# Kernel tuning notes

Measured on AMD Instinct MI355X. Metric: run time of the kernel, lower is better.

The kernel has to match this reference:

```python
import jax, jax.numpy as jnp
import numpy as np
from itertools import permutations

N_SOURCES = 5
BATCH = 524288
# All n! permutations as one-hot matrices: PERM_ONEHOT[p, i, j] = 1 iff perm p maps row i -> col j.
# Brute-force min over all permutations is exactly the Hungarian (linear_sum_assignment) optimum.
_PERMS = np.array(list(permutations(range(N_SOURCES))), dtype=np.int32)        # [120, 5]
PERM_ONEHOT = np.eye(N_SOURCES, dtype=np.float32)[_PERMS]                      # [120, 5, 5]


def setup_inputs() -> dict:
    key = jax.random.key(0)
    k1, k2 = jax.random.split(key)
    doa_predictions = jax.random.normal(k1, (BATCH, N_SOURCES), dtype=jnp.float32)
    doa_targets = jax.random.normal(k2, (BATCH, N_SOURCES), dtype=jnp.float32)
    return {"doa_predictions": doa_predictions, "doa_targets": doa_targets}


def reference(doa_predictions, doa_targets):
    n = doa_predictions.shape[1]
    # pairwise mod-pi differences, wrapped into [-pi/2, pi/2): [B, n_pred, n_tgt]
    diff = doa_predictions[:, :, None] - doa_targets[:, None, :]
    diff = (diff + jnp.pi / 2) % jnp.pi - jnp.pi / 2
    cost = diff * diff                                                   # [B, n, n]
    # total squared error under each permutation: [B, P]
    perm_costs = jnp.einsum('bij,pij->bp', cost, jnp.asarray(PERM_ONEHOT))
    min_cost = jnp.min(perm_costs, axis=1)                               # optimal assignment cost per sample
    rmspe = jnp.sqrt(min_cost / n)
    return jnp.sum(rmspe)
```

## Files before the change

kernel.cpp:

```cpp
#include <hip/hip_runtime.h>
#include <math.h>


#define NSRC 5

__device__ __forceinline__ float sample_rmspe(const float pr[NSRC], const float tg[NSRC]) {
    const float PI     = 3.14159265358979323846f;
    const float INV_PI = 0.31830988618379067154f;

    float c[NSRC][NSRC];
#pragma unroll
    for (int i = 0; i < NSRC; ++i) {
#pragma unroll
        for (int j = 0; j < NSRC; ++j) {
            float x = pr[i] - tg[j];
            float d = x - PI * floorf(fmaf(x, INV_PI, 0.5f));
            c[i][j] = d * d;
        }
    }

    float dp[1 << NSRC];
    dp[0] = 0.0f;
#pragma unroll
    for (int mask = 1; mask < (1 << NSRC); ++mask) {
        const int i = __popc(mask) - 1;
        float best = 3.4e38f;
#pragma unroll
        for (int j = 0; j < NSRC; ++j) {
            if (mask & (1 << j)) {
                float cand = dp[mask ^ (1 << j)] + c[i][j];
                best = fminf(best, cand);
            }
        }
        dp[mask] = best;
    }
    return sqrtf(dp[(1 << NSRC) - 1] * (1.0f / NSRC));
}

__global__ __launch_bounds__(256) void rmspe_partial(const float4* __restrict__ pred4,
                                                     const float4* __restrict__ tgt4,
                                                     float* __restrict__ partial,
                                                     int nquad, int B,
                                                     const float* __restrict__ pred,
                                                     const float* __restrict__ tgt) {
    float val = 0.0f;
    const int stride = gridDim.x * blockDim.x;
    for (int q = blockIdx.x * blockDim.x + threadIdx.x; q < nquad; q += stride) {
        const float4* pp = pred4 + (size_t)q * NSRC;
        const float4* tp = tgt4  + (size_t)q * NSRC;
        float4 p0 = pp[0], p1 = pp[1], p2 = pp[2], p3 = pp[3], p4 = pp[4];
        float4 t0 = tp[0], t1 = tp[1], t2 = tp[2], t3 = tp[3], t4 = tp[4];
        float pf[20] = {p0.x,p0.y,p0.z,p0.w, p1.x,p1.y,p1.z,p1.w,
                        p2.x,p2.y,p2.z,p2.w, p3.x,p3.y,p3.z,p3.w,
                        p4.x,p4.y,p4.z,p4.w};
        float tf[20] = {t0.x,t0.y,t0.z,t0.w, t1.x,t1.y,t1.z,t1.w,
                        t2.x,t2.y,t2.z,t2.w, t3.x,t3.y,t3.z,t3.w,
                        t4.x,t4.y,t4.z,t4.w};
#pragma unroll
        for (int s = 0; s < 4; ++s)
            val += sample_rmspe(&pf[s * NSRC], &tf[s * NSRC]);
    }

    const int tail_start = nquad * 4;
    const int gtid = blockIdx.x * blockDim.x + threadIdx.x;
    if (tail_start + gtid < B) {
        float pr[NSRC], tg[NSRC];
#pragma unroll
        for (int i = 0; i < NSRC; ++i) {
            pr[i] = pred[(size_t)(tail_start + gtid) * NSRC + i];
            tg[i] = tgt [(size_t)(tail_start + gtid) * NSRC + i];
        }
        val += sample_rmspe(pr, tg);
    }

#pragma unroll
    for (int off = 32; off > 0; off >>= 1)
        val += __shfl_down(val, off, 64);

    __shared__ float wsum[4];
    const int lane = threadIdx.x & 63;
    const int wid  = threadIdx.x >> 6;
    if (lane == 0) wsum[wid] = val;
    __syncthreads();
    if (threadIdx.x == 0)
        partial[blockIdx.x] = wsum[0] + wsum[1] + wsum[2] + wsum[3];
}

__global__ __launch_bounds__(256) void rmspe_reduce(const float* __restrict__ partial,
                                                    int n, float* __restrict__ out) {
    float v = 0.0f;
    for (int i = threadIdx.x; i < n; i += 256) v += partial[i];
#pragma unroll
    for (int off = 32; off > 0; off >>= 1)
        v += __shfl_down(v, off, 64);
    __shared__ float wsum[4];
    const int lane = threadIdx.x & 63;
    const int wid  = threadIdx.x >> 6;
    if (lane == 0) wsum[wid] = v;
    __syncthreads();
    if (threadIdx.x == 0)
        out[0] = wsum[0] + wsum[1] + wsum[2] + wsum[3];
}

extern "C" void kernel_launch(void* const* d_in, const int* in_sizes, int n_in,
                              void* d_out, int out_size, void* d_ws, size_t ws_size,
                              hipStream_t stream) {
    const float* pred = (const float*)d_in[0];
    const float* tgt  = (const float*)d_in[1];
    float* out = (float*)d_out;
    float* partial = (float*)d_ws;

    const int B = in_sizes[0] / NSRC;
    const int nquad = B / 4;

    const int threads = 256;
    int blocks = (nquad + threads - 1) / threads;
    if (blocks > 2048) blocks = 2048;
    if (blocks < 1) blocks = 1;

    rmspe_partial<<<blocks, threads, 0, stream>>>(
        (const float4*)pred, (const float4*)tgt, partial, nquad, B, pred, tgt);
    rmspe_reduce<<<1, threads, 0, stream>>>(partial, blocks, out);
}
```

Measured before the change: 11.86 us.

## Prescale inputs by 1/pi and wrap with hardware fract; shrink grid and reducer

Inputs are pre-scaled by 1/pi once per element, with the +0.5 offset folded into predictions, so each of the 25 pairwise wraps becomes a hardware fract minus 0.5. The squared-cost scale (pi^2/n) moves into a single multiply before a native sqrt per sample. This removes per-pair floor and multiply work from the ALU-bound inner loop. The grid is capped at 512 blocks so each thread handles more quads, and the final reducer becomes a single wave with no shared memory. Fract-based wrapping may differ slightly in rounding from the floor-based modulo near wrap boundaries.

```diff
diff --git a/kernel.cpp b/kernel.cpp
--- a/kernel.cpp
+++ b/kernel.cpp
@@ -4,18 +4,15 @@
 
 #define NSRC 5
 
-__device__ __forceinline__ float sample_rmspe(const float pr[NSRC], const float tg[NSRC]) {
-    const float PI     = 3.14159265358979323846f;
-    const float INV_PI = 0.31830988618379067154f;
-
+__device__ __forceinline__ float sample_dp(const float u[NSRC], const float v[NSRC]) {
     float c[NSRC][NSRC];
 #pragma unroll
     for (int i = 0; i < NSRC; ++i) {
 #pragma unroll
         for (int j = 0; j < NSRC; ++j) {
-            float x = pr[i] - tg[j];
-            float d = x - PI * floorf(fmaf(x, INV_PI, 0.5f));
-            c[i][j] = d * d;
+            float t = u[i] - v[j];
+            float g = __builtin_amdgcn_fractf(t) - 0.5f;
+            c[i][j] = g * g;
         }
     }
 
@@ -34,7 +31,7 @@
         }
         dp[mask] = best;
     }
-    return sqrtf(dp[(1 << NSRC) - 1] * (1.0f / NSRC));
+    return dp[(1 << NSRC) - 1];
 }
 
 __global__ __launch_bounds__(256) void rmspe_partial(const float4* __restrict__ pred4,
@@ -43,6 +40,9 @@
                                                      int nquad, int B,
                                                      const float* __restrict__ pred,
                                                      const float* __restrict__ tgt) {
+    const float INV_PI = 0.31830988618379067154f;
+    const float PI2_OVER_N = 1.9739208802178717f;
+
     float val = 0.0f;
     const int stride = gridDim.x * blockDim.x;
     for (int q = blockIdx.x * blockDim.x + threadIdx.x; q < nquad; q += stride) {
@@ -57,20 +57,27 @@
                         t2.x,t2.y,t2.z,t2.w, t3.x,t3.y,t3.z,t3.w,
                         t4.x,t4.y,t4.z,t4.w};
 #pragma unroll
-        for (int s = 0; s < 4; ++s)
-            val += sample_rmspe(&pf[s * NSRC], &tf[s * NSRC]);
+        for (int k = 0; k < 20; ++k) {
+            pf[k] = fmaf(pf[k], INV_PI, 0.5f);
+            tf[k] = tf[k] * INV_PI;
+        }
+#pragma unroll
+        for (int s = 0; s < 4; ++s) {
+            float m = sample_dp(&pf[s * NSRC], &tf[s * NSRC]);
+            val += __builtin_amdgcn_sqrtf(m * PI2_OVER_N);
+        }
     }
 
     const int tail_start = nquad * 4;
     const int gtid = blockIdx.x * blockDim.x + threadIdx.x;
     if (tail_start + gtid < B) {
-        float pr[NSRC], tg[NSRC];
+        float u[NSRC], v[NSRC];
 #pragma unroll
         for (int i = 0; i < NSRC; ++i) {
-            pr[i] = pred[(size_t)(tail_start + gtid) * NSRC + i];
-            tg[i] = tgt [(size_t)(tail_start + gtid) * NSRC + i];
+            u[i] = fmaf(pred[(size_t)(tail_start + gtid) * NSRC + i], INV_PI, 0.5f);
+            v[i] = tgt [(size_t)(tail_start + gtid) * NSRC + i] * INV_PI;
         }
-        val += sample_rmspe(pr, tg);
+        val += __builtin_amdgcn_sqrtf(sample_dp(u, v) * PI2_OVER_N);
     }
 
 #pragma unroll
@@ -86,20 +93,14 @@
         partial[blockIdx.x] = wsum[0] + wsum[1] + wsum[2] + wsum[3];
 }
 
-__global__ __launch_bounds__(256) void rmspe_reduce(const float* __restrict__ partial,
-                                                    int n, float* __restrict__ out) {
+__global__ __launch_bounds__(64) void rmspe_reduce(const float* __restrict__ partial,
+                                                   int n, float* __restrict__ out) {
     float v = 0.0f;
-    for (int i = threadIdx.x; i < n; i += 256) v += partial[i];
+    for (int i = threadIdx.x; i < n; i += 64) v += partial[i];
 #pragma unroll
     for (int off = 32; off > 0; off >>= 1)
         v += __shfl_down(v, off, 64);
-    __shared__ float wsum[4];
-    const int lane = threadIdx.x & 63;
-    const int wid  = threadIdx.x >> 6;
-    if (lane == 0) wsum[wid] = v;
-    __syncthreads();
-    if (threadIdx.x == 0)
-        out[0] = wsum[0] + wsum[1] + wsum[2] + wsum[3];
+    if (threadIdx.x == 0) out[0] = v;
 }
 
 extern "C" void kernel_launch(void* const* d_in, const int* in_sizes, int n_in,
@@ -115,10 +116,10 @@
 
     const int threads = 256;
     int blocks = (nquad + threads - 1) / threads;
-    if (blocks > 2048) blocks = 2048;
+    if (blocks > 512) blocks = 512;
     if (blocks < 1) blocks = 1;
 
     rmspe_partial<<<blocks, threads, 0, stream>>>(
         (const float4*)pred, (const float4*)tgt, partial, nquad, B, pred, tgt);
-    rmspe_reduce<<<1, threads, 0, stream>>>(partial, blocks, out);
+    rmspe_reduce<<<1, 64, 0, stream>>>(partial, blocks, out);
 }
```

Result: slower. 13.46 us (+13.5%).
